# Performance work log

Measured on AMD Instinct MI355X. Metric: run time of the kernel, lower is better.

## Reference

```python
import jax, jax.numpy as jnp
import numpy as np

B, S, D, H, C = 64, 512, 768, 768, 5


def setup_inputs() -> dict:
    key = jax.random.key(0)
    ks = jax.random.split(key, 7)
    return {
        "hidden_states": jax.random.normal(ks[0], (B, S, D), jnp.float32),
        "mask": jnp.ones((B, S), dtype=bool),
        # Dense(hidden_size, relu)
        "W1": jax.random.normal(ks[1], (D, H), jnp.float32) * 0.02,
        "b1": jnp.zeros((H,), jnp.float32),
        # CRF inner dense -> potentials over num_classes
        "W2": jax.random.normal(ks[2], (H, C), jnp.float32) * 0.02,
        "b2": jnp.zeros((C,), jnp.float32),
        # CRF transition matrix and boundary energies (tfa use_boundary=True)
        "chain_kernel": jax.random.normal(ks[3], (C, C), jnp.float32) * 0.1,
        "left_boundary": jax.random.normal(ks[4], (C,), jnp.float32) * 0.1,
        "right_boundary": jax.random.normal(ks[5], (C,), jnp.float32) * 0.1,
    }


def viterbi_decode(potentials, trans):
    """potentials: [B,S,C], trans: [C,C] -> decoded tags [B,S] int32."""
    pot_t = jnp.swapaxes(potentials, 0, 1)  # [S,B,C]

    def fwd_step(alpha, pot):
        scores = alpha[:, :, None] + trans[None]      # [B,C_prev,C_cur]
        bp = jnp.argmax(scores, axis=1)               # [B,C]
        alpha = jnp.max(scores, axis=1) + pot         # [B,C]
        return alpha, bp

    alpha, bps = jax.lax.scan(fwd_step, pot_t[0], pot_t[1:])  # bps: [S-1,B,C]
    last = jnp.argmax(alpha, axis=-1).astype(jnp.int32)       # [B]

    def back_step(tag, bp):
        prev = jnp.take_along_axis(bp, tag[:, None], axis=1)[:, 0].astype(jnp.int32)
        return prev, prev

    _, tags = jax.lax.scan(back_step, last, bps, reverse=True)  # [S-1,B]
    decoded = jnp.concatenate([jnp.swapaxes(tags, 0, 1), last[:, None]], axis=1)
    return decoded


def reference(hidden_states, mask, W1, b1, W2, b2, chain_kernel,
              left_boundary, right_boundary):
    # Dense + ReLU (dropout is identity at inference / training=False)
    h = jax.nn.relu(jnp.einsum('bsd,dh->bsh', hidden_states, W1) + b1)
    # CRF inner dense -> unary potentials
    pot = jnp.einsum('bsh,hc->bsc', h, W2) + b2
    # boundary energies at first / last timestep (mask is full-length here)
    pot = pot.at[:, 0].add(left_boundary).at[:, -1].add(right_boundary)
    seq_length = jnp.sum(mask.astype(jnp.int32), axis=1)
    decoded = viterbi_decode(pot, chain_kernel)
    return decoded, pot, seq_length, chain_kernel
```

## Files before the change

kernel.cpp:

```cpp
#include <hip/hip_runtime.h>

#define B_  64
#define S_  512
#define D_  768
#define H_  768
#define C_  5
#define M_  (B_ * S_)

typedef float f32x4 __attribute__((ext_vector_type(4)));
typedef short short8 __attribute__((ext_vector_type(8)));

#define W1T_ELEMS (D_ * H_)
#define XBF_ELEMS (M_ * D_)

__device__ __forceinline__ unsigned short f2bf(float f) {
    unsigned int u = __float_as_uint(f);
    u += 0x7FFFu + ((u >> 16) & 1u);
    return (unsigned short)(u >> 16);
}

__global__ __launch_bounds__(256) void init_pot_kernel(
    const float* __restrict__ b2, const float* __restrict__ lb,
    const float* __restrict__ rb, float* __restrict__ pot)
{
    const int idx = blockIdx.x * 256 + threadIdx.x;
    if (idx < M_ * C_) {
        const int c = idx % C_;
        const int t = (idx / C_) & (S_ - 1);
        float v = b2[c];
        if (t == 0)      v += lb[c];
        if (t == S_ - 1) v += rb[c];
        pot[idx] = v;
    }
}

__global__ __launch_bounds__(256) void prep_w1_kernel(
    const float* __restrict__ W1, unsigned short* __restrict__ w1t)
{
    __shared__ float t[32][33];
    const int bx = blockIdx.x;
    const int by = blockIdx.y;
    const int lx = threadIdx.x & 31, ly = threadIdx.x >> 5;
    #pragma unroll
    for (int j = 0; j < 4; ++j)
        t[ly + 8 * j][lx] = W1[(by * 32 + ly + 8 * j) * H_ + bx * 32 + lx];
    __syncthreads();
    #pragma unroll
    for (int j = 0; j < 4; ++j)
        w1t[(size_t)(bx * 32 + ly + 8 * j) * D_ + by * 32 + lx] = f2bf(t[lx][ly + 8 * j]);
}

__global__ __launch_bounds__(256) void prep_x_kernel(
    const float* __restrict__ X, unsigned short* __restrict__ xbf)
{
    const size_t i0 = ((size_t)blockIdx.x * 256 + threadIdx.x) * 8;
    const float4 a = *(const float4*)(X + i0);
    const float4 b = *(const float4*)(X + i0 + 4);
    union { unsigned short u[8]; uint4 v; } o;
    o.u[0] = f2bf(a.x); o.u[1] = f2bf(a.y); o.u[2] = f2bf(a.z); o.u[3] = f2bf(a.w);
    o.u[4] = f2bf(b.x); o.u[5] = f2bf(b.y); o.u[6] = f2bf(b.z); o.u[7] = f2bf(b.w);
    *(uint4*)(xbf + i0) = o.v;
}

__device__ __forceinline__ void gload16(const void* g, void* l) {
    __builtin_amdgcn_global_load_lds(
        (const __attribute__((address_space(1))) unsigned int*)g,
        (__attribute__((address_space(3))) unsigned int*)l, 16, 0, 0);
}

__global__ __launch_bounds__(256) void gemm_bf16x2_kernel(
    const unsigned short* __restrict__ xbf,
    const unsigned short* __restrict__ w1t,
    const float* __restrict__ b1,
    const float* __restrict__ W2,
    float* __restrict__ pot)
{
    __shared__ __align__(16) unsigned short Asm[128 * 32];
    __shared__ __align__(16) unsigned short Bsm[128 * 32];
    __shared__ float pp[2][128][C_];

    const int tid  = threadIdx.x;
    const int lane = tid & 63, w = tid >> 6;
    const int wm   = w >> 1, wn = w & 1;
    const int i15  = lane & 15, quad = lane >> 4;

    const int bid = blockIdx.x;
    const int r8 = bid & 7, q8 = bid >> 3;
    const int nb = q8 % 6, mhi = q8 / 6;
    const int m0 = (mhi * 8 + r8) * 128;
    const int n0 = nb * 128;

    const unsigned short* gA[2];
    const unsigned short* gB[2];
    unsigned short* lA[2];
    unsigned short* lB[2];
    #pragma unroll
    for (int i = 0; i < 2; ++i) {
        const int g = 2 * w + i;
        gA[i] = xbf + (size_t)(m0 + g * 16 + i15) * D_ + quad * 8;
        lA[i] = &Asm[g * 512];
        gB[i] = w1t + (size_t)(n0 + g * 16 + i15) * D_ + quad * 8;
        lB[i] = &Bsm[g * 512];
    }

    f32x4 acc[4][4];
    #pragma unroll
    for (int mi = 0; mi < 4; ++mi)
        #pragma unroll
        for (int ni = 0; ni < 4; ++ni)
            acc[mi][ni] = (f32x4){0.f, 0.f, 0.f, 0.f};

    for (int kt = 0; kt < D_ / 32; ++kt) {
        __syncthreads();
        #pragma unroll
        for (int i = 0; i < 2; ++i) { gload16(gA[i], lA[i]); gA[i] += 32; }
        #pragma unroll
        for (int i = 0; i < 2; ++i) { gload16(gB[i], lB[i]); gB[i] += 32; }
        __syncthreads();

        short8 af[4], bfr[4];
        #pragma unroll
        for (int mi = 0; mi < 4; ++mi)
            af[mi] = *(const short8*)&Asm[(wm * 4 + mi) * 512 + quad * 128 + i15 * 8];
        #pragma unroll
        for (int ni = 0; ni < 4; ++ni)
            bfr[ni] = *(const short8*)&Bsm[(wn * 4 + ni) * 512 + quad * 128 + i15 * 8];

        #pragma unroll
        for (int ni = 0; ni < 4; ++ni)
            #pragma unroll
            for (int mi = 0; mi < 4; ++mi)
                acc[mi][ni] = __builtin_amdgcn_mfma_f32_16x16x32_bf16(
                    af[mi], bfr[ni], acc[mi][ni], 0, 0, 0);
    }

    float b1v[4], w2v[4][C_];
    #pragma unroll
    for (int ni = 0; ni < 4; ++ni) {
        const int col = n0 + wn * 64 + ni * 16 + i15;
        b1v[ni] = b1[col];
        #pragma unroll
        for (int cc = 0; cc < C_; ++cc) w2v[ni][cc] = W2[col * C_ + cc];
    }

    #pragma unroll
    for (int mi = 0; mi < 4; ++mi) {
        float ps[4][C_];
        #pragma unroll
        for (int r = 0; r < 4; ++r)
            #pragma unroll
            for (int cc = 0; cc < C_; ++cc) ps[r][cc] = 0.f;

        #pragma unroll
        for (int ni = 0; ni < 4; ++ni)
            #pragma unroll
            for (int r = 0; r < 4; ++r) {
                float h = acc[mi][ni][r] + b1v[ni];
                h = h > 0.f ? h : 0.f;
                #pragma unroll
                for (int cc = 0; cc < C_; ++cc)
                    ps[r][cc] = fmaf(h, w2v[ni][cc], ps[r][cc]);
            }

        #pragma unroll
        for (int off = 1; off < 16; off <<= 1)
            #pragma unroll
            for (int r = 0; r < 4; ++r)
                #pragma unroll
                for (int cc = 0; cc < C_; ++cc)
                    ps[r][cc] += __shfl_xor(ps[r][cc], off, 64);

        if (i15 == 0) {
            #pragma unroll
            for (int r = 0; r < 4; ++r) {
                const int row = wm * 64 + mi * 16 + quad * 4 + r;
                #pragma unroll
                for (int cc = 0; cc < C_; ++cc)
                    pp[wn][row][cc] = ps[r][cc];
            }
        }
    }
    __syncthreads();

    for (int idx = tid; idx < 128 * C_; idx += 256) {
        const int row = idx / C_, cc = idx % C_;
        atomicAdd(&pot[(size_t)(m0 + row) * C_ + cc],
                  pp[0][row][cc] + pp[1][row][cc]);
    }
}

__global__ __launch_bounds__(256) void gemm_bf16_kernel(
    const float* __restrict__ X,
    const unsigned short* __restrict__ w1t,
    const float* __restrict__ b1,
    const float* __restrict__ W2,
    float* __restrict__ pot)
{
    __shared__ __align__(16) float          Asm[128 * 32];
    __shared__ __align__(16) unsigned short Bsm[128 * 32];
    __shared__ float pp[2][128][C_];

    const int tid  = threadIdx.x;
    const int lane = tid & 63, w = tid >> 6;
    const int wm   = w >> 1, wn = w & 1;
    const int i15  = lane & 15, quad = lane >> 4;

    const int bid = blockIdx.x;
    const int r8 = bid & 7, q8 = bid >> 3;
    const int nb = q8 % 6, mhi = q8 / 6;
    const int m0 = (mhi * 8 + r8) * 128;
    const int n0 = nb * 128;

    const float* gA[4];
    float* lA[4];
    const unsigned short* gB[2];
    unsigned short* lB[2];
    #pragma unroll
    for (int i = 0; i < 4; ++i) {
        const int a = 4 * w + i, g = a >> 1, h = a & 1;
        gA[i] = X + (size_t)(m0 + g * 16 + i15) * D_ + (4 * h + quad) * 4;
        lA[i] = &Asm[g * 512 + h * 256];
    }
    #pragma unroll
    for (int i = 0; i < 2; ++i) {
        const int b = 2 * w + i;
        gB[i] = w1t + (size_t)(n0 + b * 16 + i15) * D_ + quad * 8;
        lB[i] = &Bsm[b * 512];
    }

    f32x4 acc[4][4];
    #pragma unroll
    for (int mi = 0; mi < 4; ++mi)
        #pragma unroll
        for (int ni = 0; ni < 4; ++ni)
            acc[mi][ni] = (f32x4){0.f, 0.f, 0.f, 0.f};

    for (int kt = 0; kt < D_ / 32; ++kt) {
        __syncthreads();
        #pragma unroll
        for (int i = 0; i < 4; ++i) { gload16(gA[i], lA[i]); gA[i] += 32; }
        #pragma unroll
        for (int i = 0; i < 2; ++i) { gload16(gB[i], lB[i]); gB[i] += 32; }
        __syncthreads();

        short8 af[4];
        #pragma unroll
        for (int mi = 0; mi < 4; ++mi) {
            const int row = wm * 64 + mi * 16 + i15;
            const int base = (row >> 4) * 512 + (row & 15) * 4 + quad * 128;
            const f32x4 lo = *(const f32x4*)&Asm[base];
            const f32x4 hi = *(const f32x4*)&Asm[base + 64];
            float f[8];
            *(f32x4*)&f[0] = lo; *(f32x4*)&f[4] = hi;
            union { short8 s; unsigned short u[8]; } cv;
            #pragma unroll
            for (int j = 0; j < 8; ++j) cv.u[j] = f2bf(f[j]);
            af[mi] = cv.s;
        }
        short8 bfr[4];
        #pragma unroll
        for (int ni = 0; ni < 4; ++ni) {
            const int row = wn * 64 + ni * 16 + i15;
            bfr[ni] = *(const short8*)&Bsm[(row >> 4) * 512 + quad * 128 + (row & 15) * 8];
        }
        #pragma unroll
        for (int ni = 0; ni < 4; ++ni)
            #pragma unroll
            for (int mi = 0; mi < 4; ++mi)
                acc[mi][ni] = __builtin_amdgcn_mfma_f32_16x16x32_bf16(
                    af[mi], bfr[ni], acc[mi][ni], 0, 0, 0);
    }

    float b1v[4], w2v[4][C_];
    #pragma unroll
    for (int ni = 0; ni < 4; ++ni) {
        const int col = n0 + wn * 64 + ni * 16 + i15;
        b1v[ni] = b1[col];
        #pragma unroll
        for (int cc = 0; cc < C_; ++cc) w2v[ni][cc] = W2[col * C_ + cc];
    }

    #pragma unroll
    for (int mi = 0; mi < 4; ++mi) {
        float ps[4][C_];
        #pragma unroll
        for (int r = 0; r < 4; ++r)
            #pragma unroll
            for (int cc = 0; cc < C_; ++cc) ps[r][cc] = 0.f;

        #pragma unroll
        for (int ni = 0; ni < 4; ++ni)
            #pragma unroll
            for (int r = 0; r < 4; ++r) {
                float h = acc[mi][ni][r] + b1v[ni];
                h = h > 0.f ? h : 0.f;
                #pragma unroll
                for (int cc = 0; cc < C_; ++cc)
                    ps[r][cc] = fmaf(h, w2v[ni][cc], ps[r][cc]);
            }

        #pragma unroll
        for (int off = 1; off < 16; off <<= 1)
            #pragma unroll
            for (int r = 0; r < 4; ++r)
                #pragma unroll
                for (int cc = 0; cc < C_; ++cc)
                    ps[r][cc] += __shfl_xor(ps[r][cc], off, 64);

        if (i15 == 0) {
            #pragma unroll
            for (int r = 0; r < 4; ++r) {
                const int row = wm * 64 + mi * 16 + quad * 4 + r;
                #pragma unroll
                for (int cc = 0; cc < C_; ++cc)
                    pp[wn][row][cc] = ps[r][cc];
            }
        }
    }
    __syncthreads();

    for (int idx = tid; idx < 128 * C_; idx += 256) {
        const int row = idx / C_, cc = idx % C_;
        atomicAdd(&pot[(size_t)(m0 + row) * C_ + cc],
                  pp[0][row][cc] + pp[1][row][cc]);
    }
}

#define FBK 8
#define FLDS 132
__global__ __launch_bounds__(256) void gemm_relu_pot_kernel(
    const float* __restrict__ X, const float* __restrict__ W1,
    const float* __restrict__ b1, const float* __restrict__ W2,
    float* __restrict__ pot)
{
    __shared__ float As[FBK * FLDS];
    __shared__ float Bs[FBK * FLDS];
    __shared__ float w2s[128][C_];

    const int tid = threadIdx.x;
    const int tx = tid & 15, ty = tid >> 4;
    const int m0 = blockIdx.y * 128, n0 = blockIdx.x * 128;

    for (int idx = tid; idx < 128 * C_; idx += 256)
        w2s[idx / C_][idx % C_] = W2[(n0 + idx / C_) * C_ + idx % C_];

    float acc[2][2][4][4];
    #pragma unroll
    for (int a = 0; a < 2; ++a)
        #pragma unroll
        for (int b = 0; b < 2; ++b)
            #pragma unroll
            for (int i = 0; i < 4; ++i)
                #pragma unroll
                for (int j = 0; j < 4; ++j) acc[a][b][i][j] = 0.f;

    const int arow = tid >> 1, aq = tid & 1;
    const int brow = tid >> 5, bq = tid & 31;
    const float* Aptr = X + (m0 + arow) * D_ + aq * 4;
    const float* Bptr = W1 + brow * H_ + n0 + bq * 4;

    for (int kt = 0; kt < D_; kt += FBK) {
        const float4 avv = *(const float4*)Aptr;
        const float4 bvv = *(const float4*)Bptr;
        __syncthreads();
        As[(aq * 4 + 0) * FLDS + arow] = avv.x;
        As[(aq * 4 + 1) * FLDS + arow] = avv.y;
        As[(aq * 4 + 2) * FLDS + arow] = avv.z;
        As[(aq * 4 + 3) * FLDS + arow] = avv.w;
        *(float4*)&Bs[brow * FLDS + bq * 4] = bvv;
        __syncthreads();
        #pragma unroll
        for (int k = 0; k < FBK; ++k) {
            const float4 a0 = *(const float4*)&As[k * FLDS + (ty << 2)];
            const float4 a1 = *(const float4*)&As[k * FLDS + 64 + (ty << 2)];
            const float4 b0 = *(const float4*)&Bs[k * FLDS + (tx << 2)];
            const float4 b1r = *(const float4*)&Bs[k * FLDS + 64 + (tx << 2)];
            const float ar[2][4] = {{a0.x,a0.y,a0.z,a0.w},{a1.x,a1.y,a1.z,a1.w}};
            const float br[2][4] = {{b0.x,b0.y,b0.z,b0.w},{b1r.x,b1r.y,b1r.z,b1r.w}};
            #pragma unroll
            for (int ri = 0; ri < 2; ++ri)
                #pragma unroll
                for (int i = 0; i < 4; ++i)
                    #pragma unroll
                    for (int rj = 0; rj < 2; ++rj)
                        #pragma unroll
                        for (int j = 0; j < 4; ++j)
                            acc[ri][rj][i][j] = fmaf(ar[ri][i], br[rj][j], acc[ri][rj][i][j]);
        }
        Aptr += FBK;
        Bptr += FBK * H_;
    }

    float ps[2][4][C_];
    #pragma unroll
    for (int ri = 0; ri < 2; ++ri)
        #pragma unroll
        for (int i = 0; i < 4; ++i)
            #pragma unroll
            for (int cc = 0; cc < C_; ++cc) ps[ri][i][cc] = 0.f;

    #pragma unroll
    for (int rj = 0; rj < 2; ++rj)
        #pragma unroll
        for (int j = 0; j < 4; ++j) {
            const int nl = rj * 64 + (tx << 2) + j;
            const float bj = b1[n0 + nl];
            float w2c[C_];
            #pragma unroll
            for (int cc = 0; cc < C_; ++cc) w2c[cc] = w2s[nl][cc];
            #pragma unroll
            for (int ri = 0; ri < 2; ++ri)
                #pragma unroll
                for (int i = 0; i < 4; ++i) {
                    float h = acc[ri][rj][i][j] + bj;
                    h = h > 0.f ? h : 0.f;
                    #pragma unroll
                    for (int cc = 0; cc < C_; ++cc)
                        ps[ri][i][cc] = fmaf(h, w2c[cc], ps[ri][i][cc]);
                }
        }

    #pragma unroll
    for (int off = 1; off < 16; off <<= 1)
        #pragma unroll
        for (int ri = 0; ri < 2; ++ri)
            #pragma unroll
            for (int i = 0; i < 4; ++i)
                #pragma unroll
                for (int cc = 0; cc < C_; ++cc)
                    ps[ri][i][cc] += __shfl_xor(ps[ri][i][cc], off, 64);

    if (tx == 0)
        #pragma unroll
        for (int ri = 0; ri < 2; ++ri)
            #pragma unroll
            for (int i = 0; i < 4; ++i) {
                const int m = m0 + ri * 64 + (ty << 2) + i;
                #pragma unroll
                for (int cc = 0; cc < C_; ++cc)
                    atomicAdd(&pot[m * C_ + cc], ps[ri][i][cc]);
            }
}

__global__ __launch_bounds__(64) void viterbi_kernel(
    const float* __restrict__ pot, const float* __restrict__ trans,
    const int* __restrict__ mask, float* __restrict__ decoded,
    float* __restrict__ seqlen, float* __restrict__ chain_out)
{
    const int b = blockIdx.x;
    const int lane = threadIdx.x;

    __shared__ float pl[S_ * C_];
    __shared__ unsigned int bpk[S_];
    __shared__ unsigned int gseg[64];
    __shared__ int bt[64];
    __shared__ int dec_s[S_];
    __shared__ int s_last;

    const float* pb = pot + b * (S_ * C_);
    for (int i = lane; i < S_ * C_; i += 64) pl[i] = pb[i];

    int mcnt = 0;
    const int* mb = mask + b * S_;
    for (int i = lane; i < S_; i += 64) mcnt += (mb[i] != 0) ? 1 : 0;
    #pragma unroll
    for (int off = 32; off >= 1; off >>= 1) mcnt += __shfl_xor(mcnt, off, 64);

    if (b == 0 && lane < C_ * C_) chain_out[lane] = trans[lane];

    float tr[C_][C_];
    #pragma unroll
    for (int p = 0; p < C_; ++p)
        #pragma unroll
        for (int c = 0; c < C_; ++c) tr[p][c] = trans[p * C_ + c];

    __syncthreads();

    const float NEG = -1.0e30f;

    float G[C_][C_];
    #pragma unroll
    for (int c = 0; c < C_; ++c)
        #pragma unroll
        for (int p = 0; p < C_; ++p) G[c][p] = (c == p) ? 0.f : NEG;

    for (int j = 1; j <= 8; ++j) {
        const int t = 8 * lane + j;
        if (t < S_) {
            float ng[C_][C_];
            #pragma unroll
            for (int c = 0; c < C_; ++c) {
                const float pc = pl[t * C_ + c];
                #pragma unroll
                for (int p = 0; p < C_; ++p) {
                    float m = tr[0][c] + G[0][p];
                    #pragma unroll
                    for (int q = 1; q < C_; ++q)
                        m = fmaxf(m, tr[q][c] + G[q][p]);
                    ng[c][p] = m + pc;
                }
            }
            #pragma unroll
            for (int c = 0; c < C_; ++c)
                #pragma unroll
                for (int p = 0; p < C_; ++p) G[c][p] = ng[c][p];
        }
    }

    #pragma unroll
    for (int d = 1; d < 64; d <<= 1) {
        float Q[C_][C_];
        #pragma unroll
        for (int q = 0; q < C_; ++q)
            #pragma unroll
            for (int p = 0; p < C_; ++p) Q[q][p] = __shfl_up(G[q][p], d, 64);
        if (lane >= d) {
            float ng[C_][C_];
            #pragma unroll
            for (int c = 0; c < C_; ++c)
                #pragma unroll
                for (int p = 0; p < C_; ++p) {
                    float m = G[c][0] + Q[0][p];
                    #pragma unroll
                    for (int q = 1; q < C_; ++q)
                        m = fmaxf(m, G[c][q] + Q[q][p]);
                    ng[c][p] = m;
                }
            #pragma unroll
            for (int c = 0; c < C_; ++c)
                #pragma unroll
                for (int p = 0; p < C_; ++p) G[c][p] = ng[c][p];
        }
    }

    float a[C_];
    {
        float E[C_][C_];
        #pragma unroll
        for (int c = 0; c < C_; ++c)
            #pragma unroll
            for (int p = 0; p < C_; ++p) E[c][p] = __shfl_up(G[c][p], 1, 64);
        float a0[C_];
        #pragma unroll
        for (int c = 0; c < C_; ++c) a0[c] = pl[c];
        if (lane == 0) {
            #pragma unroll
            for (int c = 0; c < C_; ++c) a[c] = a0[c];
        } else {
            #pragma unroll
            for (int c = 0; c < C_; ++c) {
                float m = E[c][0] + a0[0];
                #pragma unroll
                for (int q = 1; q < C_; ++q) m = fmaxf(m, E[c][q] + a0[q]);
                a[c] = m;
            }
        }
    }

    for (int j = 1; j <= 8; ++j) {
        const int t = 8 * lane + j;
        if (t < S_) {
            unsigned int mpack = 0;
            float na[C_];
            #pragma unroll
            for (int c = 0; c < C_; ++c) {
                float best = a[0] + tr[0][c];
                int arg = 0;
                #pragma unroll
                for (int p = 1; p < C_; ++p) {
                    const float s = a[p] + tr[p][c];
                    if (s > best) { best = s; arg = p; }
                }
                mpack |= (unsigned int)arg << (3 * c);
                na[c] = best + pl[t * C_ + c];
            }
            bpk[t] = mpack;
            #pragma unroll
            for (int c = 0; c < C_; ++c) a[c] = na[c];
        }
    }

    if (lane == 63) {
        float best = a[0];
        int arg = 0;
        #pragma unroll
        for (int p = 1; p < C_; ++p)
            if (a[p] > best) { best = a[p]; arg = p; }
        s_last = arg;
    }
    if (lane == 0) bpk[0] = 0;
    __syncthreads();

    const int last = s_last;

    unsigned int g = 0u | (1u << 3) | (2u << 6) | (3u << 9) | (4u << 12);
    #pragma unroll
    for (int j = 7; j >= 0; --j) {
        const int t = 8 * lane + j;
        if (t >= 1) {
            const unsigned int m = bpk[t];
            unsigned int ng = 0;
            #pragma unroll
            for (int x = 0; x < C_; ++x) {
                const unsigned int gx = (g >> (3 * x)) & 7u;
                ng |= ((m >> (3 * gx)) & 7u) << (3 * x);
            }
            g = ng;
        }
    }
    gseg[lane] = g;
    __syncthreads();

    if (lane == 0) {
        int cur = last;
        for (int l = 63; l >= 0; --l) {
            bt[l] = cur;
            cur = (int)((gseg[l] >> (3 * cur)) & 7u);
        }
        seqlen[b] = (float)mcnt;
    }
    __syncthreads();

    {
        int tag = bt[lane];
        const int t0 = 8 * lane;
        dec_s[t0 + 7] = tag;
        #pragma unroll
        for (int t = t0 + 7; t >= t0 + 1; --t) {
            tag = (int)((bpk[t] >> (3 * tag)) & 7u);
            dec_s[t - 1] = tag;
        }
    }
    __syncthreads();

    float* db = decoded + b * S_;
    for (int i = lane; i < S_; i += 64) db[i] = (float)dec_s[i];
}

extern "C" void kernel_launch(void* const* d_in, const int* in_sizes, int n_in,
                              void* d_out, int out_size, void* d_ws, size_t ws_size,
                              hipStream_t stream) {
    const float* hs    = (const float*)d_in[0];
    const int*   mask  = (const int*)  d_in[1];
    const float* W1    = (const float*)d_in[2];
    const float* b1    = (const float*)d_in[3];
    const float* W2    = (const float*)d_in[4];
    const float* b2    = (const float*)d_in[5];
    const float* chain = (const float*)d_in[6];
    const float* lb    = (const float*)d_in[7];
    const float* rb    = (const float*)d_in[8];

    float* out      = (float*)d_out;
    float* decoded  = out;
    float* pot      = out + M_;
    float* seq      = out + M_ + M_ * C_;
    float* chainout = seq + B_;

    init_pot_kernel<<<(M_ * C_ + 255) / 256, 256, 0, stream>>>(b2, lb, rb, pot);

    const size_t need_w1 = (size_t)W1T_ELEMS * sizeof(unsigned short);
    const size_t need_all = need_w1 + (size_t)XBF_ELEMS * sizeof(unsigned short);

    if (ws_size >= need_all) {
        unsigned short* w1t = (unsigned short*)d_ws;
        unsigned short* xbf = w1t + W1T_ELEMS;
        dim3 pgrid(H_ / 32, D_ / 32);
        prep_w1_kernel<<<pgrid, 256, 0, stream>>>(W1, w1t);
        prep_x_kernel<<<XBF_ELEMS / (256 * 8), 256, 0, stream>>>(hs, xbf);
        gemm_bf16x2_kernel<<<1536, 256, 0, stream>>>(xbf, w1t, b1, W2, pot);
    } else if (ws_size >= need_w1) {
        unsigned short* w1t = (unsigned short*)d_ws;
        dim3 pgrid(H_ / 32, D_ / 32);
        prep_w1_kernel<<<pgrid, 256, 0, stream>>>(W1, w1t);
        gemm_bf16_kernel<<<1536, 256, 0, stream>>>(hs, w1t, b1, W2, pot);
    } else {
        dim3 grid(H_ / 128, M_ / 128);
        gemm_relu_pot_kernel<<<grid, 256, 0, stream>>>(hs, W1, b1, W2, pot);
    }

    viterbi_kernel<<<B_, 64, 0, stream>>>(pot, chain, mask, decoded, seq, chainout);
}
```

Measured before the change: 276.4 us.

## Load GEMM operands directly into registers with software prefetch, dropping LDS staging

The bf16 GEMM stops staging A and B tiles through shared memory with global_load_lds and block-wide barriers. Each wave now loads its MFMA fragments straight from global memory into registers and prefetches the next k-slice while the current MFMAs run. This removes two __syncthreads per k-iteration and the LDS round trip. In exchange, operands shared between waves are fetched from global or L2 twice, and register pressure rises from the double-buffered fragments.

```diff
diff --git a/kernel.cpp b/kernel.cpp
--- a/kernel.cpp
+++ b/kernel.cpp
@@ -62,21 +62,13 @@
     *(uint4*)(xbf + i0) = o.v;
 }
 
-__device__ __forceinline__ void gload16(const void* g, void* l) {
-    __builtin_amdgcn_global_load_lds(
-        (const __attribute__((address_space(1))) unsigned int*)g,
-        (__attribute__((address_space(3))) unsigned int*)l, 16, 0, 0);
-}
-
-__global__ __launch_bounds__(256) void gemm_bf16x2_kernel(
+__global__ __launch_bounds__(256) void gemm_reg_kernel(
     const unsigned short* __restrict__ xbf,
     const unsigned short* __restrict__ w1t,
     const float* __restrict__ b1,
     const float* __restrict__ W2,
     float* __restrict__ pot)
 {
-    __shared__ __align__(16) unsigned short Asm[128 * 32];
-    __shared__ __align__(16) unsigned short Bsm[128 * 32];
     __shared__ float pp[2][128][C_];
 
     const int tid  = threadIdx.x;
@@ -90,18 +82,14 @@
     const int m0 = (mhi * 8 + r8) * 128;
     const int n0 = nb * 128;
 
-    const unsigned short* gA[2];
-    const unsigned short* gB[2];
-    unsigned short* lA[2];
-    unsigned short* lB[2];
-    #pragma unroll
-    for (int i = 0; i < 2; ++i) {
-        const int g = 2 * w + i;
-        gA[i] = xbf + (size_t)(m0 + g * 16 + i15) * D_ + quad * 8;
-        lA[i] = &Asm[g * 512];
-        gB[i] = w1t + (size_t)(n0 + g * 16 + i15) * D_ + quad * 8;
-        lB[i] = &Bsm[g * 512];
-    }
+    const unsigned short* pa[4];
+    const unsigned short* pb[4];
+    #pragma unroll
+    for (int mi = 0; mi < 4; ++mi)
+        pa[mi] = xbf + (size_t)(m0 + wm * 64 + mi * 16 + i15) * D_ + quad * 8;
+    #pragma unroll
+    for (int ni = 0; ni < 4; ++ni)
+        pb[ni] = w1t + (size_t)(n0 + wn * 64 + ni * 16 + i15) * D_ + quad * 8;
 
     f32x4 acc[4][4];
     #pragma unroll
@@ -110,28 +98,35 @@
         for (int ni = 0; ni < 4; ++ni)
             acc[mi][ni] = (f32x4){0.f, 0.f, 0.f, 0.f};
 
-    for (int kt = 0; kt < D_ / 32; ++kt) {
-        __syncthreads();
-        #pragma unroll
-        for (int i = 0; i < 2; ++i) { gload16(gA[i], lA[i]); gA[i] += 32; }
-        #pragma unroll
-        for (int i = 0; i < 2; ++i) { gload16(gB[i], lB[i]); gB[i] += 32; }
-        __syncthreads();
-
-        short8 af[4], bfr[4];
-        #pragma unroll
-        for (int mi = 0; mi < 4; ++mi)
-            af[mi] = *(const short8*)&Asm[(wm * 4 + mi) * 512 + quad * 128 + i15 * 8];
-        #pragma unroll
-        for (int ni = 0; ni < 4; ++ni)
-            bfr[ni] = *(const short8*)&Bsm[(wn * 4 + ni) * 512 + quad * 128 + i15 * 8];
+    short8 a_cur[4], b_cur[4];
+    #pragma unroll
+    for (int mi = 0; mi < 4; ++mi) a_cur[mi] = *(const short8*)pa[mi];
+    #pragma unroll
+    for (int ni = 0; ni < 4; ++ni) b_cur[ni] = *(const short8*)pb[ni];
+
+    #define KITERS (D_ / 32)
+    for (int kt = 0; kt < KITERS; ++kt) {
+        short8 a_nxt[4], b_nxt[4];
+        if (kt + 1 < KITERS) {
+            #pragma unroll
+            for (int mi = 0; mi < 4; ++mi) { pa[mi] += 32; a_nxt[mi] = *(const short8*)pa[mi]; }
+            #pragma unroll
+            for (int ni = 0; ni < 4; ++ni) { pb[ni] += 32; b_nxt[ni] = *(const short8*)pb[ni]; }
+        }
 
         #pragma unroll
         for (int ni = 0; ni < 4; ++ni)
             #pragma unroll
             for (int mi = 0; mi < 4; ++mi)
                 acc[mi][ni] = __builtin_amdgcn_mfma_f32_16x16x32_bf16(
-                    af[mi], bfr[ni], acc[mi][ni], 0, 0, 0);
+                    a_cur[mi], b_cur[ni], acc[mi][ni], 0, 0, 0);
+
+        if (kt + 1 < KITERS) {
+            #pragma unroll
+            for (int mi = 0; mi < 4; ++mi) a_cur[mi] = a_nxt[mi];
+            #pragma unroll
+            for (int ni = 0; ni < 4; ++ni) b_cur[ni] = b_nxt[ni];
+        }
     }
 
     float b1v[4], w2v[4][C_];
@@ -187,6 +182,12 @@
         atomicAdd(&pot[(size_t)(m0 + row) * C_ + cc],
                   pp[0][row][cc] + pp[1][row][cc]);
     }
+}
+
+__device__ __forceinline__ void gload16(const void* g, void* l) {
+    __builtin_amdgcn_global_load_lds(
+        (const __attribute__((address_space(1))) unsigned int*)g,
+        (__attribute__((address_space(3))) unsigned int*)l, 16, 0, 0);
 }
 
 __global__ __launch_bounds__(256) void gemm_bf16_kernel(
@@ -667,7 +668,7 @@
         dim3 pgrid(H_ / 32, D_ / 32);
         prep_w1_kernel<<<pgrid, 256, 0, stream>>>(W1, w1t);
         prep_x_kernel<<<XBF_ELEMS / (256 * 8), 256, 0, stream>>>(hs, xbf);
-        gemm_bf16x2_kernel<<<1536, 256, 0, stream>>>(xbf, w1t, b1, W2, pot);
+        gemm_reg_kernel<<<1536, 256, 0, stream>>>(xbf, w1t, b1, W2, pot);
     } else if (ws_size >= need_w1) {
         unsigned short* w1t = (unsigned short*)d_ws;
         dim3 pgrid(H_ / 32, D_ / 32);
```

Result: slower. 323.0 us (+16.9%).
